# Optimization experiments

Hardware: AMD Instinct MI355X
Metric: run time of the kernel (lower is better)

Reference implementation:

```python
import jax, jax.numpy as jnp
import numpy as np

B, N, C = 8, 4096, 512
NH, R = 8, 4
EPS = 1e-5

def setup_inputs() -> dict:
    key = jax.random.key(0)
    ks = jax.random.split(key, 6)
    s = lambda k, shape: jax.random.normal(k, shape, jnp.float32) * 0.02
    return {
        'x': jax.random.normal(ks[0], (B, N, C), jnp.float32),
        'Wq': s(ks[1], (C, C)), 'bq': jnp.zeros((C,), jnp.float32),
        'Wkv': s(ks[2], (C, 2 * C)), 'bkv': jnp.zeros((2 * C,), jnp.float32),
        'Wp': s(ks[3], (C, C)), 'bp': jnp.zeros((C,), jnp.float32),
        'Wsr': s(ks[4], (C, C, R, R)), 'bsr': jnp.zeros((C,), jnp.float32),
        'gamma': jnp.ones((C,), jnp.float32), 'beta': jnp.zeros((C,), jnp.float32),
        'H': 64, 'W': 64,
    }

def reference(x, Wq, bq, Wkv, bkv, Wp, bp, Wsr, bsr, gamma, beta, H, W):
    b, n, c = x.shape
    nh = NH
    hd = c // nh
    scale = hd ** -0.5
    # Q projection -> [B, nh, N, hd]
    q = (x @ Wq + bq).reshape(b, n, nh, hd).transpose(0, 2, 1, 3)
    # spatial reduction of KV input: Conv2d(k=stride=R), NCHW
    x_sp = x.transpose(0, 2, 1).reshape(b, c, H, W)
    xr = jax.lax.conv_general_dilated(
        x_sp, Wsr, window_strides=(R, R), padding='VALID',
        dimension_numbers=('NCHW', 'OIHW', 'NCHW')) + bsr[None, :, None, None]
    nr = (H // R) * (W // R)
    xr = xr.reshape(b, c, nr).transpose(0, 2, 1)  # [B, Nr, C]
    # LayerNorm over channels
    mu = xr.mean(-1, keepdims=True)
    var = xr.var(-1, keepdims=True)
    xr = (xr - mu) / jnp.sqrt(var + EPS) * gamma + beta
    # KV projection -> k, v: [B, nh, Nr, hd]
    kv = (xr @ Wkv + bkv).reshape(b, nr, 2, nh, hd)
    k = kv[:, :, 0].transpose(0, 2, 1, 3)
    v = kv[:, :, 1].transpose(0, 2, 1, 3)
    # attention
    attn = jax.nn.softmax(jnp.einsum('bhnd,bhmd->bhnm', q, k) * scale, axis=-1)
    out = jnp.einsum('bhnm,bhmd->bhnd', attn, v).transpose(0, 2, 1, 3).reshape(b, n, c)
    return out @ Wp + bp
```

## Files before the change

### kernel.cpp

```cpp
#include <hip/hip_runtime.h>
#include <stdint.h>

typedef __attribute__((ext_vector_type(8))) short bf16x8;
typedef __attribute__((ext_vector_type(4))) float f32x4;
typedef __attribute__((ext_vector_type(2))) unsigned u32x2;

#define MFMA16(a,b,c) __builtin_amdgcn_mfma_f32_16x16x32_bf16(a,b,c,0,0,0)

typedef const __attribute__((address_space(1))) void GV;
typedef __attribute__((address_space(3))) void LV;

static __device__ __forceinline__ void gload16(const void* g, void* l) {
  __builtin_amdgcn_global_load_lds((GV*)g, (LV*)l, 16, 0, 0);
}

static __device__ __forceinline__ unsigned short f2bf(float f) {
  union { float f; unsigned u; } x; x.f = f;
  unsigned r = x.u + 0x7FFFu + ((x.u >> 16) & 1u);
  return (unsigned short)(r >> 16);
}

static __device__ __forceinline__ float fast_exp2(float x) {
#if __has_builtin(__builtin_amdgcn_exp2f)
  return __builtin_amdgcn_exp2f(x);
#else
  return __expf(x * 0.6931471805599453f);
#endif
}

__global__ __launch_bounds__(256) void pack_all(
    const float* __restrict__ x, const float* __restrict__ Wq,
    const float* __restrict__ Wkv, const float* __restrict__ Wp,
    const float* __restrict__ Wsr,
    unsigned short* __restrict__ xb, unsigned short* __restrict__ wqt,
    unsigned short* __restrict__ wkvt, unsigned short* __restrict__ wpt,
    unsigned short* __restrict__ wsrt) {
  const int tid = threadIdx.x;
  int bid = blockIdx.x;
  if (bid < 16384) {
    int i = bid * 256 + tid;
    float4 v = ((const float4*)x)[i];
    unsigned a0 = f2bf(v.x), a1 = f2bf(v.y), a2 = f2bf(v.z), a3 = f2bf(v.w);
    uint2 pk; pk.x = a0 | (a1 << 16); pk.y = a2 | (a3 << 16);
    ((uint2*)xb)[i] = pk;
    return;
  }
  bid -= 16384;
  __shared__ float lsm[8704];

  auto wtile = [&](const float* __restrict__ W, unsigned short* __restrict__ out,
                   int ldw, int tr, int tc) {
    int k0 = tr * 64, n0 = tc * 64;
    #pragma unroll
    for (int i = 0; i < 16; ++i) {
      int idx = i * 256 + tid; int r = idx >> 6, c = idx & 63;
      lsm[r * 65 + c] = W[(size_t)(k0 + r) * ldw + n0 + c];
    }
    __syncthreads();
    #pragma unroll
    for (int i = 0; i < 16; ++i) {
      int idx = i * 256 + tid; int n = idx >> 6, k = idx & 63;
      out[(size_t)(n0 + n) * 512 + k0 + k] = f2bf(lsm[k * 65 + n]);
    }
  };

  if (bid < 64) { wtile(Wq, wqt, 512, bid >> 3, bid & 7); return; }
  bid -= 64;
  if (bid < 128) { wtile(Wkv, wkvt, 1024, bid >> 4, bid & 15); return; }
  bid -= 128;
  if (bid < 64) { wtile(Wp, wpt, 512, bid >> 3, bid & 7); return; }
  bid -= 64;
  int oc = bid;
  #pragma unroll
  for (int i = 0; i < 32; ++i) {
    int idx = i * 256 + tid;
    lsm[(idx >> 4) * 17 + (idx & 15)] = Wsr[(size_t)oc * 8192 + idx];
  }
  __syncthreads();
  #pragma unroll
  for (int i = 0; i < 32; ++i) {
    int idx = i * 256 + tid;
    int ic = idx & 511, r12 = idx >> 9;
    wsrt[(size_t)oc * 8192 + idx] = f2bf(lsm[ic * 17 + r12]);
  }
}

template<int WM, int WN, int MREP, int NREP, int MODE, bool CONV>
static __device__ __forceinline__ void gemm_body(
    unsigned short* lds_a, unsigned short* lds_b,
    const unsigned short* __restrict__ A, const unsigned short* __restrict__ Bt,
    const float* __restrict__ bias, void* __restrict__ outp,
    unsigned short* __restrict__ out_k, unsigned short* __restrict__ out_v,
    int M, int N, int K, int lda, int Ksub, int m0, int n0, int kbeg, int zslice) {
  constexpr int BM = WM * MREP * 16;
  constexpr int BN = WN * NREP * 16;
  constexpr int BK = 64;
  constexpr int ABYTES = BM * BK * 2;
  constexpr int BBYTES = BN * BK * 2;
  const int tid = threadIdx.x;
  const int lane = tid & 63, w = tid >> 6;
  const int wr = w / WN, wc = w % WN;
  const int l15 = lane & 15, lhi = lane >> 4;
  const int xmask = (l15 & 7) << 4;
  const int smask = ((tid >> 3) & 7) << 3;

  f32x4 acc[MREP][NREP] = {};
  constexpr int AR = ABYTES / 4096;
  constexpr int BR = BBYTES / 4096;
  constexpr int NL = AR + BR;

  auto stage = [&](int buf, int k0) {
    #pragma unroll
    for (int r = 0; r < AR; ++r) {
      int o = r * 4096 + tid * 16;
      int row = o >> 7;
      int kc = (((o & 127) >> 1)) ^ smask;
      const unsigned short* src;
      if constexpr (CONV) {
        int m = m0 + row;
        int bb = m >> 8, pix = m & 255;
        int oh = pix >> 4, ow = pix & 15;
        int r12 = k0 >> 9;
        int icc = (k0 & 511) + kc;
        int r1 = r12 >> 2, r2 = r12 & 3;
        int nn = (oh * 4 + r1) * 64 + ow * 4 + r2;
        src = A + ((size_t)(bb * 4096 + nn)) * 512 + icc;
      } else {
        src = A + (size_t)(m0 + row) * lda + k0 + kc;
      }
      gload16(src, (char*)lds_a + buf * ABYTES + r * 4096 + w * 1024);
    }
    #pragma unroll
    for (int r = 0; r < BR; ++r) {
      int o = r * 4096 + tid * 16;
      int row = o >> 7;
      int kc = (((o & 127) >> 1)) ^ smask;
      const unsigned short* src = Bt + (size_t)(n0 + row) * K + k0 + kc;
      gload16(src, (char*)lds_b + buf * BBYTES + r * 4096 + w * 1024);
    }
  };

  auto waitn = [&]() {
    if constexpr (NL == 4)      asm volatile("s_waitcnt vmcnt(4)" ::: "memory");
    else if constexpr (NL == 6) asm volatile("s_waitcnt vmcnt(6)" ::: "memory");
    else                        asm volatile("s_waitcnt vmcnt(8)" ::: "memory");
  };

  auto compute = [&](int buf) {
    const char* pa = (const char*)lds_a + buf * ABYTES;
    const char* pb = (const char*)lds_b + buf * BBYTES;
    #pragma unroll
    for (int kk = 0; kk < BK; kk += 32) {
      bf16x8 af[MREP], bfr[NREP];
      #pragma unroll
      for (int m = 0; m < MREP; ++m)
        af[m] = *(const bf16x8*)(pa + (wr * MREP * 16 + m * 16 + l15) * (BK * 2)
                                 + (((kk << 1) + (lhi << 4)) ^ xmask));
      #pragma unroll
      for (int n = 0; n < NREP; ++n)
        bfr[n] = *(const bf16x8*)(pb + (wc * NREP * 16 + n * 16 + l15) * (BK * 2)
                                  + (((kk << 1) + (lhi << 4)) ^ xmask));
      __builtin_amdgcn_s_setprio(1);
      #pragma unroll
      for (int m = 0; m < MREP; ++m)
        #pragma unroll
        for (int n = 0; n < NREP; ++n)
          acc[m][n] = MFMA16(af[m], bfr[n], acc[m][n]);
      __builtin_amdgcn_s_setprio(0);
    }
  };

  const int nsteps = Ksub / BK;
  stage(0, kbeg);
  int buf = 0;
  for (int t = 0; t < nsteps; ++t) {
    if (t + 1 < nsteps) {
      stage(buf ^ 1, kbeg + (t + 1) * BK);
      waitn();
    } else {
      asm volatile("s_waitcnt vmcnt(0)" ::: "memory");
    }
    __builtin_amdgcn_s_barrier();
    compute(buf);
    __builtin_amdgcn_s_barrier();
    buf ^= 1;
  }

  #pragma unroll
  for (int m = 0; m < MREP; ++m) {
    #pragma unroll
    for (int n = 0; n < NREP; ++n) {
      #pragma unroll
      for (int r = 0; r < 4; ++r) {
        int gm = m0 + wr * MREP * 16 + m * 16 + lhi * 4 + r;
        int gn = n0 + wc * NREP * 16 + n * 16 + l15;
        if constexpr (MODE == 0) {
          float v = acc[m][n][r] + bias[gn];
          ((float*)outp)[(size_t)gm * N + gn] = v;
        } else if constexpr (MODE == 3) {
          ((float*)outp)[((size_t)zslice * M + gm) * N + gn] = acc[m][n][r];
        } else if constexpr (MODE == 4) {
          float v = (acc[m][n][r] + bias[gn]) * 0.18033688011112042f;
          int b_ = gm >> 12, n_ = gm & 4095;
          int hh = gn >> 6, d = gn & 63;
          int qt = n_ >> 4, half = d >> 5, dd = d & 31;
          int ln = (n_ & 15) | ((dd >> 3) << 4);
          ((unsigned short*)outp)[(size_t)(b_ * 8 + hh) * 262144 +
              (qt * 2 + half) * 512 + ln * 8 + (d & 7)] = f2bf(v);
        } else {
          float v = acc[m][n][r] + bias[gn];
          unsigned short bv = f2bf(v);
          int bb = gm >> 8, nr = gm & 255;
          if (gn < 512) {
            int hh = gn >> 6, d = gn & 63;
            int t_ = nr >> 4, half = d >> 5, dd = d & 31;
            int ln = (nr & 15) | ((dd >> 3) << 4);
            out_k[(size_t)(bb * 8 + hh) * 16384 +
                  (t_ * 2 + half) * 512 + ln * 8 + (d & 7)] = bv;
          } else {
            int c = gn - 512;
            int hh = c >> 6, d = c & 63;
            int nn = d >> 4, cl = d & 15;
            int ks = nr >> 5, lh = (nr >> 3) & 3;
            out_v[(size_t)(bb * 8 + hh) * 16384 +
                  (nn * 8 + ks) * 512 + (cl | (lh << 4)) * 8 + (nr & 7)] = bv;
          }
        }
      }
    }
  }
}

template<int WM, int WN, int MREP, int NREP, int MODE, bool CONV, bool SWZ>
__global__ __launch_bounds__(256) void gemm_bf16(
    const unsigned short* __restrict__ A, const unsigned short* __restrict__ Bt,
    const float* __restrict__ bias, void* __restrict__ outp,
    unsigned short* __restrict__ out_k, unsigned short* __restrict__ out_v,
    int M, int N, int K, int lda, int Ksub) {
  constexpr int BM = WM * MREP * 16;
  constexpr int BN = WN * NREP * 16;
  __shared__ unsigned short lds_a[2 * BM * 64];
  __shared__ unsigned short lds_b[2 * BN * 64];
  int mt, nt_;
  if constexpr (SWZ) {
    int lin = blockIdx.x + blockIdx.y * gridDim.x;
    int nwg = gridDim.x * gridDim.y;
    int cpx = nwg >> 3;
    int s = (lin & 7) * cpx + (lin >> 3);
    int gdy = gridDim.y;
    mt = s / gdy; nt_ = s - mt * gdy;
  } else { mt = blockIdx.x; nt_ = blockIdx.y; }
  gemm_body<WM, WN, MREP, NREP, MODE, CONV>(
      lds_a, lds_b, A, Bt, bias, outp, out_k, out_v,
      M, N, K, lda, Ksub, mt * BM, nt_ * BN, blockIdx.z * Ksub, blockIdx.z);
}

__global__ __launch_bounds__(256) void proj_fused(
    const unsigned short* __restrict__ xb, const unsigned short* __restrict__ wqt,
    const float* __restrict__ bq, unsigned short* __restrict__ qfrag,
    const unsigned short* __restrict__ xln, const unsigned short* __restrict__ wkvt,
    const float* __restrict__ bkv, unsigned short* __restrict__ kfrag,
    unsigned short* __restrict__ vfrag) {
  __shared__ unsigned short lds_a[2 * 128 * 64];
  __shared__ unsigned short lds_b[2 * 128 * 64];
  int bx = blockIdx.x;
  if (bx < 1024) {
    int s = (bx & 7) * 128 + (bx >> 3);
    int mt = s >> 2, nt_ = s & 3;
    gemm_body<2, 2, 4, 4, 4, false>(
        lds_a, lds_b, xb, wqt, bq, qfrag, nullptr, nullptr,
        32768, 512, 512, 512, 512, mt * 128, nt_ * 128, 0, 0);
  } else {
    int b2 = bx - 1024;
    int mt = b2 >> 3, nt_ = b2 & 7;
    gemm_body<2, 2, 4, 4, 2, false>(
        lds_a, lds_b, xln, wkvt, bkv, nullptr, kfrag, vfrag,
        2048, 1024, 512, 512, 512, mt * 128, nt_ * 128, 0, 0);
  }
}

__global__ __launch_bounds__(64) void ln_kernel(
    const float* __restrict__ part, const float* __restrict__ bsr,
    const float* __restrict__ gamma, const float* __restrict__ beta,
    unsigned short* __restrict__ xln) {
  const int row = blockIdx.x, lane = threadIdx.x;
  float vv[8];
  #pragma unroll
  for (int j = 0; j < 8; ++j) vv[j] = bsr[lane * 8 + j];
  #pragma unroll
  for (int p = 0; p < 8; ++p) {
    const float* pp = part + ((size_t)p * 2048 + row) * 512 + lane * 8;
    float4 a0 = *(const float4*)pp;
    float4 a1 = *(const float4*)(pp + 4);
    vv[0] += a0.x; vv[1] += a0.y; vv[2] += a0.z; vv[3] += a0.w;
    vv[4] += a1.x; vv[5] += a1.y; vv[6] += a1.z; vv[7] += a1.w;
  }
  float s = 0.f, s2 = 0.f;
  #pragma unroll
  for (int j = 0; j < 8; ++j) { s += vv[j]; s2 += vv[j] * vv[j]; }
  #pragma unroll
  for (int m_ = 1; m_ < 64; m_ <<= 1) { s += __shfl_xor(s, m_); s2 += __shfl_xor(s2, m_); }
  float mean = s * (1.f / 512.f);
  float var = s2 * (1.f / 512.f) - mean * mean;
  float inv = rsqrtf(var + 1e-5f);
  #pragma unroll
  for (int j = 0; j < 8; ++j) {
    int c = lane * 8 + j;
    xln[(size_t)row * 512 + c] = f2bf((vv[j] - mean) * inv * gamma[c] + beta[c]);
  }
}

__global__ __launch_bounds__(512, 4) void attn_kernel(
    const unsigned short* __restrict__ qfrag, const unsigned short* __restrict__ kfrag,
    const unsigned short* __restrict__ vfrag, unsigned short* __restrict__ aout) {
  __shared__ unsigned short k_lds[16384];
  __shared__ unsigned short v_lds[16384];
  const int tid = threadIdx.x, lane = tid & 63, w = tid >> 6;
  const int l15 = lane & 15;
  const int b = blockIdx.z, h = blockIdx.y;
  const int bh = b * 8 + h;
  const char* kb_ = (const char*)(kfrag + (size_t)bh * 16384);
  const char* vb_ = (const char*)(vfrag + (size_t)bh * 16384);
  #pragma unroll
  for (int r = 0; r < 4; ++r) {
    gload16(kb_ + r * 8192 + tid * 16, (char*)k_lds + r * 8192 + w * 1024);
    gload16(vb_ + r * 8192 + tid * 16, (char*)v_lds + r * 8192 + w * 1024);
  }
  const int qt = blockIdx.x * 8 + w;
  const unsigned short* qbase = qfrag + (size_t)bh * 262144 + (size_t)qt * 1024;
  bf16x8 qf0 = *(const bf16x8*)(qbase + lane * 8);
  bf16x8 qf1 = *(const bf16x8*)(qbase + 512 + lane * 8);
  __syncthreads();

  f32x4 st[16];
  #pragma unroll
  for (int t = 0; t < 16; ++t) {
    bf16x8 kf0 = *(const bf16x8*)&k_lds[t * 1024 + lane * 8];
    bf16x8 kf1 = *(const bf16x8*)&k_lds[t * 1024 + 512 + lane * 8];
    f32x4 a = {0.f, 0.f, 0.f, 0.f};
    a = MFMA16(kf0, qf0, a);
    a = MFMA16(kf1, qf1, a);
    st[t] = a;
  }

  float sum = 0.f;
  unsigned pk2[16][2];
  #pragma unroll
  for (int t = 0; t < 16; ++t) {
    float p0 = fast_exp2(st[t][0]), p1 = fast_exp2(st[t][1]);
    float p2 = fast_exp2(st[t][2]), p3 = fast_exp2(st[t][3]);
    sum += (p0 + p1) + (p2 + p3);
    unsigned r0, r1;
    asm("v_cvt_pk_bf16_f32 %0, %1, %2" : "=v"(r0) : "v"(p0), "v"(p1));
    asm("v_cvt_pk_bf16_f32 %0, %1, %2" : "=v"(r1) : "v"(p2), "v"(p3));
    pk2[t][0] = r0; pk2[t][1] = r1;
  }
  sum += __shfl_xor(sum, 16);
  sum += __shfl_xor(sum, 32);
  float invs = 1.f / sum;

  const int lhi_ = lane >> 4;
  const int srcA = l15 + (((2 * lhi_) & 3) << 4);
  const int srcB = l15 + (((2 * lhi_ + 1) & 3) << 4);
  const bool hi2 = lhi_ >= 2;
  f32x4 o[4] = {};
  #pragma unroll
  for (int ks = 0; ks < 8; ++ks) {
    union { unsigned u[4]; bf16x8 v; } pu;
    unsigned A0 = __shfl(pk2[2 * ks][0], srcA),     A0b = __shfl(pk2[2 * ks][1], srcA);
    unsigned A1 = __shfl(pk2[2 * ks + 1][0], srcA), A1b = __shfl(pk2[2 * ks + 1][1], srcA);
    unsigned B0 = __shfl(pk2[2 * ks][0], srcB),     B0b = __shfl(pk2[2 * ks][1], srcB);
    unsigned B1 = __shfl(pk2[2 * ks + 1][0], srcB), B1b = __shfl(pk2[2 * ks + 1][1], srcB);
    pu.u[0] = hi2 ? A1 : A0;  pu.u[1] = hi2 ? A1b : A0b;
    pu.u[2] = hi2 ? B1 : B0;  pu.u[3] = hi2 ? B1b : B0b;
    #pragma unroll
    for (int n = 0; n < 4; ++n) {
      bf16x8 vf = *(const bf16x8*)&v_lds[(n * 8 + ks) * 512 + lane * 8];
      o[n] = MFMA16(vf, pu.v, o[n]);
    }
  }

  const int q0 = blockIdx.x * 128;
  const int lhi = lane >> 4;
  #pragma unroll
  for (int n = 0; n < 4; ++n) {
    float a0 = o[n][0] * invs, a1 = o[n][1] * invs;
    float a2 = o[n][2] * invs, a3 = o[n][3] * invs;
    unsigned w0, w1;
    asm("v_cvt_pk_bf16_f32 %0, %1, %2" : "=v"(w0) : "v"(a0), "v"(a1));
    asm("v_cvt_pk_bf16_f32 %0, %1, %2" : "=v"(w1) : "v"(a2), "v"(a3));
    u32x2 pr; pr[0] = w0; pr[1] = w1;
    size_t base = (size_t)(b * 4096 + q0 + w * 16 + l15) * 512 + h * 64 + n * 16 + lhi * 4;
    *(u32x2*)(aout + base) = pr;
  }
}

extern "C" void kernel_launch(void* const* d_in, const int* in_sizes, int n_in,
                              void* d_out, int out_size, void* d_ws, size_t ws_size,
                              hipStream_t stream) {
  const float* x     = (const float*)d_in[0];
  const float* Wq    = (const float*)d_in[1];
  const float* bq    = (const float*)d_in[2];
  const float* Wkv   = (const float*)d_in[3];
  const float* bkv   = (const float*)d_in[4];
  const float* Wp    = (const float*)d_in[5];
  const float* bp    = (const float*)d_in[6];
  const float* Wsr   = (const float*)d_in[7];
  const float* bsr   = (const float*)d_in[8];
  const float* gamma = (const float*)d_in[9];
  const float* beta  = (const float*)d_in[10];

  char* ws = (char*)d_ws;
  unsigned short* xb    = (unsigned short*)(ws + 0);
  float*          part  = (float*)(ws + 33554432);
  unsigned short* qfrag = (unsigned short*)(ws + 33554432);
  unsigned short* wqt   = (unsigned short*)(ws + 67108864);
  unsigned short* wkvt  = (unsigned short*)(ws + 67633152);
  unsigned short* wpt   = (unsigned short*)(ws + 68681728);
  unsigned short* wsrt  = (unsigned short*)(ws + 69206016);
  unsigned short* xln   = (unsigned short*)(ws + 77594624);
  unsigned short* kfrag = (unsigned short*)(ws + 79691776);
  unsigned short* vfrag = (unsigned short*)(ws + 81788928);
  unsigned short* aout  = xb;

  pack_all<<<17152, 256, 0, stream>>>(x, Wq, Wkv, Wp, Wsr, xb, wqt, wkvt, wpt, wsrt);
  gemm_bf16<2, 2, 4, 4, 3, true, true><<<dim3(16, 4, 8), 256, 0, stream>>>(
      xb, wsrt, nullptr, part, nullptr, nullptr, 2048, 512, 8192, 512, 1024);
  ln_kernel<<<2048, 64, 0, stream>>>(part, bsr, gamma, beta, xln);
  proj_fused<<<1152, 256, 0, stream>>>(xb, wqt, bq, qfrag, xln, wkvt, bkv, kfrag, vfrag);
  attn_kernel<<<dim3(32, 8, 8), 512, 0, stream>>>(qfrag, kfrag, vfrag, aout);
  gemm_bf16<2, 2, 4, 4, 0, false, true><<<dim3(256, 4, 1), 256, 0, stream>>>(
      aout, wpt, bp, (float*)d_out, nullptr, nullptr, 32768, 512, 512, 512, 512);
}
```

Before: 154.3 us.

## Replace double-buffered LDS staging with single buffer in GEMM body

Removes the double-buffered global-to-LDS prefetch in the shared GEMM body, so each K step now loads a tile, waits for all loads to finish, computes, and then syncs. LDS allocation is halved, which could allow more workgroups per CU. In exchange, global load latency is no longer overlapped with MFMA compute within a workgroup.

```diff
diff --git a/kernel.cpp b/kernel.cpp
--- a/kernel.cpp
+++ b/kernel.cpp
@@ -107,9 +107,8 @@
   f32x4 acc[MREP][NREP] = {};
   constexpr int AR = ABYTES / 4096;
   constexpr int BR = BBYTES / 4096;
-  constexpr int NL = AR + BR;
-
-  auto stage = [&](int buf, int k0) {
+
+  auto stage = [&](int k0) {
     #pragma unroll
     for (int r = 0; r < AR; ++r) {
       int o = r * 4096 + tid * 16;
@@ -128,7 +127,7 @@
       } else {
         src = A + (size_t)(m0 + row) * lda + k0 + kc;
       }
-      gload16(src, (char*)lds_a + buf * ABYTES + r * 4096 + w * 1024);
+      gload16(src, (char*)lds_a + r * 4096 + w * 1024);
     }
     #pragma unroll
     for (int r = 0; r < BR; ++r) {
@@ -136,19 +135,13 @@
       int row = o >> 7;
       int kc = (((o & 127) >> 1)) ^ smask;
       const unsigned short* src = Bt + (size_t)(n0 + row) * K + k0 + kc;
-      gload16(src, (char*)lds_b + buf * BBYTES + r * 4096 + w * 1024);
+      gload16(src, (char*)lds_b + r * 4096 + w * 1024);
     }
   };
 
-  auto waitn = [&]() {
-    if constexpr (NL == 4)      asm volatile("s_waitcnt vmcnt(4)" ::: "memory");
-    else if constexpr (NL == 6) asm volatile("s_waitcnt vmcnt(6)" ::: "memory");
-    else                        asm volatile("s_waitcnt vmcnt(8)" ::: "memory");
-  };
-
-  auto compute = [&](int buf) {
-    const char* pa = (const char*)lds_a + buf * ABYTES;
-    const char* pb = (const char*)lds_b + buf * BBYTES;
+  auto compute = [&]() {
+    const char* pa = (const char*)lds_a;
+    const char* pb = (const char*)lds_b;
     #pragma unroll
     for (int kk = 0; kk < BK; kk += 32) {
       bf16x8 af[MREP], bfr[NREP];
@@ -171,19 +164,12 @@
   };
 
   const int nsteps = Ksub / BK;
-  stage(0, kbeg);
-  int buf = 0;
   for (int t = 0; t < nsteps; ++t) {
-    if (t + 1 < nsteps) {
-      stage(buf ^ 1, kbeg + (t + 1) * BK);
-      waitn();
-    } else {
-      asm volatile("s_waitcnt vmcnt(0)" ::: "memory");
-    }
+    stage(kbeg + t * BK);
+    asm volatile("s_waitcnt vmcnt(0)" ::: "memory");
     __builtin_amdgcn_s_barrier();
-    compute(buf);
+    compute();
     __builtin_amdgcn_s_barrier();
-    buf ^= 1;
   }
 
   #pragma unroll
@@ -239,8 +225,8 @@
     int M, int N, int K, int lda, int Ksub) {
   constexpr int BM = WM * MREP * 16;
   constexpr int BN = WN * NREP * 16;
-  __shared__ unsigned short lds_a[2 * BM * 64];
-  __shared__ unsigned short lds_b[2 * BN * 64];
+  __shared__ unsigned short lds_a[BM * 64];
+  __shared__ unsigned short lds_b[BN * 64];
   int mt, nt_;
   if constexpr (SWZ) {
     int lin = blockIdx.x + blockIdx.y * gridDim.x;
@@ -261,8 +247,8 @@
     const unsigned short* __restrict__ xln, const unsigned short* __restrict__ wkvt,
     const float* __restrict__ bkv, unsigned short* __restrict__ kfrag,
     unsigned short* __restrict__ vfrag) {
-  __shared__ unsigned short lds_a[2 * 128 * 64];
-  __shared__ unsigned short lds_b[2 * 128 * 64];
+  __shared__ unsigned short lds_a[128 * 64];
+  __shared__ unsigned short lds_b[128 * 64];
   int bx = blockIdx.x;
   if (bx < 1024) {
     int s = (bx & 7) * 128 + (bx >> 3);
```

Result: slower. 167.0 us (+8.3%).

## Use single-buffered high-occupancy GEMM for projections and split fused proj kernel

Applied to the files above, without the earlier changes.

Replaces the double-buffered templated GEMM for the K=512 projections with a single-buffered kernel that uses half the LDS and sets launch_bounds(256,4), so more workgroups fit per CU and latency is hidden by occupancy instead of software pipelining. The conv GEMM keeps its own specialised double-buffered kernel. The fused Q/KV projection launch is split into two separate launches (KV first, then Q). Exposed load latency per K step and an extra kernel launch are the costs.

```diff
diff --git a/kernel.cpp b/kernel.cpp
--- a/kernel.cpp
+++ b/kernel.cpp
@@ -85,107 +85,11 @@
   }
 }
 
-template<int WM, int WN, int MREP, int NREP, int MODE, bool CONV>
-static __device__ __forceinline__ void gemm_body(
-    unsigned short* lds_a, unsigned short* lds_b,
-    const unsigned short* __restrict__ A, const unsigned short* __restrict__ Bt,
-    const float* __restrict__ bias, void* __restrict__ outp,
+template<int MREP, int NREP, int MODE>
+static __device__ __forceinline__ void epilogue(
+    f32x4 (&acc)[MREP][NREP], const float* __restrict__ bias, void* __restrict__ outp,
     unsigned short* __restrict__ out_k, unsigned short* __restrict__ out_v,
-    int M, int N, int K, int lda, int Ksub, int m0, int n0, int kbeg, int zslice) {
-  constexpr int BM = WM * MREP * 16;
-  constexpr int BN = WN * NREP * 16;
-  constexpr int BK = 64;
-  constexpr int ABYTES = BM * BK * 2;
-  constexpr int BBYTES = BN * BK * 2;
-  const int tid = threadIdx.x;
-  const int lane = tid & 63, w = tid >> 6;
-  const int wr = w / WN, wc = w % WN;
-  const int l15 = lane & 15, lhi = lane >> 4;
-  const int xmask = (l15 & 7) << 4;
-  const int smask = ((tid >> 3) & 7) << 3;
-
-  f32x4 acc[MREP][NREP] = {};
-  constexpr int AR = ABYTES / 4096;
-  constexpr int BR = BBYTES / 4096;
-  constexpr int NL = AR + BR;
-
-  auto stage = [&](int buf, int k0) {
-    #pragma unroll
-    for (int r = 0; r < AR; ++r) {
-      int o = r * 4096 + tid * 16;
-      int row = o >> 7;
-      int kc = (((o & 127) >> 1)) ^ smask;
-      const unsigned short* src;
-      if constexpr (CONV) {
-        int m = m0 + row;
-        int bb = m >> 8, pix = m & 255;
-        int oh = pix >> 4, ow = pix & 15;
-        int r12 = k0 >> 9;
-        int icc = (k0 & 511) + kc;
-        int r1 = r12 >> 2, r2 = r12 & 3;
-        int nn = (oh * 4 + r1) * 64 + ow * 4 + r2;
-        src = A + ((size_t)(bb * 4096 + nn)) * 512 + icc;
-      } else {
-        src = A + (size_t)(m0 + row) * lda + k0 + kc;
-      }
-      gload16(src, (char*)lds_a + buf * ABYTES + r * 4096 + w * 1024);
-    }
-    #pragma unroll
-    for (int r = 0; r < BR; ++r) {
-      int o = r * 4096 + tid * 16;
-      int row = o >> 7;
-      int kc = (((o & 127) >> 1)) ^ smask;
-      const unsigned short* src = Bt + (size_t)(n0 + row) * K + k0 + kc;
-      gload16(src, (char*)lds_b + buf * BBYTES + r * 4096 + w * 1024);
-    }
-  };
-
-  auto waitn = [&]() {
-    if constexpr (NL == 4)      asm volatile("s_waitcnt vmcnt(4)" ::: "memory");
-    else if constexpr (NL == 6) asm volatile("s_waitcnt vmcnt(6)" ::: "memory");
-    else                        asm volatile("s_waitcnt vmcnt(8)" ::: "memory");
-  };
-
-  auto compute = [&](int buf) {
-    const char* pa = (const char*)lds_a + buf * ABYTES;
-    const char* pb = (const char*)lds_b + buf * BBYTES;
-    #pragma unroll
-    for (int kk = 0; kk < BK; kk += 32) {
-      bf16x8 af[MREP], bfr[NREP];
-      #pragma unroll
-      for (int m = 0; m < MREP; ++m)
-        af[m] = *(const bf16x8*)(pa + (wr * MREP * 16 + m * 16 + l15) * (BK * 2)
-                                 + (((kk << 1) + (lhi << 4)) ^ xmask));
-      #pragma unroll
-      for (int n = 0; n < NREP; ++n)
-        bfr[n] = *(const bf16x8*)(pb + (wc * NREP * 16 + n * 16 + l15) * (BK * 2)
-                                  + (((kk << 1) + (lhi << 4)) ^ xmask));
-      __builtin_amdgcn_s_setprio(1);
-      #pragma unroll
-      for (int m = 0; m < MREP; ++m)
-        #pragma unroll
-        for (int n = 0; n < NREP; ++n)
-          acc[m][n] = MFMA16(af[m], bfr[n], acc[m][n]);
-      __builtin_amdgcn_s_setprio(0);
-    }
-  };
-
-  const int nsteps = Ksub / BK;
-  stage(0, kbeg);
-  int buf = 0;
-  for (int t = 0; t < nsteps; ++t) {
-    if (t + 1 < nsteps) {
-      stage(buf ^ 1, kbeg + (t + 1) * BK);
-      waitn();
-    } else {
-      asm volatile("s_waitcnt vmcnt(0)" ::: "memory");
-    }
-    __builtin_amdgcn_s_barrier();
-    compute(buf);
-    __builtin_amdgcn_s_barrier();
-    buf ^= 1;
-  }
-
+    int M, int N, int m0, int n0, int wr, int wc, int l15, int lhi, int zslice) {
   #pragma unroll
   for (int m = 0; m < MREP; ++m) {
     #pragma unroll
@@ -195,8 +99,7 @@
         int gm = m0 + wr * MREP * 16 + m * 16 + lhi * 4 + r;
         int gn = n0 + wc * NREP * 16 + n * 16 + l15;
         if constexpr (MODE == 0) {
-          float v = acc[m][n][r] + bias[gn];
-          ((float*)outp)[(size_t)gm * N + gn] = v;
+          ((float*)outp)[(size_t)gm * N + gn] = acc[m][n][r] + bias[gn];
         } else if constexpr (MODE == 3) {
           ((float*)outp)[((size_t)zslice * M + gm) * N + gn] = acc[m][n][r];
         } else if constexpr (MODE == 4) {
@@ -231,16 +134,20 @@
   }
 }
 
-template<int WM, int WN, int MREP, int NREP, int MODE, bool CONV, bool SWZ>
-__global__ __launch_bounds__(256) void gemm_bf16(
+template<int MODE, bool SWZ>
+__global__ __launch_bounds__(256, 4) void gemm_1b(
     const unsigned short* __restrict__ A, const unsigned short* __restrict__ Bt,
     const float* __restrict__ bias, void* __restrict__ outp,
     unsigned short* __restrict__ out_k, unsigned short* __restrict__ out_v,
-    int M, int N, int K, int lda, int Ksub) {
-  constexpr int BM = WM * MREP * 16;
-  constexpr int BN = WN * NREP * 16;
-  __shared__ unsigned short lds_a[2 * BM * 64];
-  __shared__ unsigned short lds_b[2 * BN * 64];
+    int M, int N, int K, int lda) {
+  constexpr int BM = 128, BN = 128, BK = 64;
+  __shared__ unsigned short lds_a[BM * BK];
+  __shared__ unsigned short lds_b[BN * BK];
+  const int tid = threadIdx.x;
+  const int lane = tid & 63, w = tid >> 6;
+  const int wr = w >> 1, wc = w & 1;
+  const int l15 = lane & 15, lhi = lane >> 4;
+  const int xmask = (l15 & 7) << 4;
   int mt, nt_;
   if constexpr (SWZ) {
     int lin = blockIdx.x + blockIdx.y * gridDim.x;
@@ -250,33 +157,143 @@
     int gdy = gridDim.y;
     mt = s / gdy; nt_ = s - mt * gdy;
   } else { mt = blockIdx.x; nt_ = blockIdx.y; }
-  gemm_body<WM, WN, MREP, NREP, MODE, CONV>(
-      lds_a, lds_b, A, Bt, bias, outp, out_k, out_v,
-      M, N, K, lda, Ksub, mt * BM, nt_ * BN, blockIdx.z * Ksub, blockIdx.z);
-}
-
-__global__ __launch_bounds__(256) void proj_fused(
-    const unsigned short* __restrict__ xb, const unsigned short* __restrict__ wqt,
-    const float* __restrict__ bq, unsigned short* __restrict__ qfrag,
-    const unsigned short* __restrict__ xln, const unsigned short* __restrict__ wkvt,
-    const float* __restrict__ bkv, unsigned short* __restrict__ kfrag,
-    unsigned short* __restrict__ vfrag) {
-  __shared__ unsigned short lds_a[2 * 128 * 64];
-  __shared__ unsigned short lds_b[2 * 128 * 64];
-  int bx = blockIdx.x;
-  if (bx < 1024) {
-    int s = (bx & 7) * 128 + (bx >> 3);
-    int mt = s >> 2, nt_ = s & 3;
-    gemm_body<2, 2, 4, 4, 4, false>(
-        lds_a, lds_b, xb, wqt, bq, qfrag, nullptr, nullptr,
-        32768, 512, 512, 512, 512, mt * 128, nt_ * 128, 0, 0);
-  } else {
-    int b2 = bx - 1024;
-    int mt = b2 >> 3, nt_ = b2 & 7;
-    gemm_body<2, 2, 4, 4, 2, false>(
-        lds_a, lds_b, xln, wkvt, bkv, nullptr, kfrag, vfrag,
-        2048, 1024, 512, 512, 512, mt * 128, nt_ * 128, 0, 0);
-  }
+  const int m0 = mt * BM;
+  const int n0 = nt_ * BN;
+
+  const int srow = tid >> 3;
+  const int kcs = ((tid & 7) << 3) ^ (((tid >> 3) & 7) << 3);
+  const unsigned short* ap = A + (size_t)(m0 + srow) * lda + kcs;
+  const unsigned short* bp = Bt + (size_t)(n0 + srow) * K + kcs;
+  char* adst = (char*)lds_a + w * 1024 + (lane << 4);
+  char* bdst = (char*)lds_b + w * 1024 + (lane << 4);
+  (void)adst; (void)bdst;
+
+  f32x4 acc[4][4] = {};
+  const int nsteps = K / BK;
+  for (int t = 0; t < nsteps; ++t) {
+    #pragma unroll
+    for (int r = 0; r < 4; ++r)
+      gload16(ap + (size_t)r * 32 * lda, (char*)lds_a + r * 4096 + w * 1024);
+    #pragma unroll
+    for (int r = 0; r < 4; ++r)
+      gload16(bp + (size_t)r * 32 * K, (char*)lds_b + r * 4096 + w * 1024);
+    asm volatile("s_waitcnt vmcnt(0)" ::: "memory");
+    __builtin_amdgcn_s_barrier();
+    #pragma unroll
+    for (int kk = 0; kk < BK; kk += 32) {
+      bf16x8 af[4], bfr[4];
+      #pragma unroll
+      for (int m = 0; m < 4; ++m)
+        af[m] = *(const bf16x8*)((const char*)lds_a + (wr * 64 + m * 16 + l15) * 128
+                                 + (((kk << 1) + (lhi << 4)) ^ xmask));
+      #pragma unroll
+      for (int n = 0; n < 4; ++n)
+        bfr[n] = *(const bf16x8*)((const char*)lds_b + (wc * 64 + n * 16 + l15) * 128
+                                  + (((kk << 1) + (lhi << 4)) ^ xmask));
+      #pragma unroll
+      for (int m = 0; m < 4; ++m)
+        #pragma unroll
+        for (int n = 0; n < 4; ++n)
+          acc[m][n] = MFMA16(af[m], bfr[n], acc[m][n]);
+    }
+    __builtin_amdgcn_s_barrier();
+    ap += BK; bp += BK;
+  }
+
+  epilogue<4, 4, MODE>(acc, bias, outp, out_k, out_v, M, N, m0, n0, wr, wc, l15, lhi, 0);
+}
+
+__global__ __launch_bounds__(256) void gemm_conv(
+    const unsigned short* __restrict__ A, const unsigned short* __restrict__ Bt,
+    float* __restrict__ outp, int Ksub) {
+  constexpr int BM = 128, BN = 128, BK = 64;
+  constexpr int ABYTES = BM * BK * 2;
+  __shared__ unsigned short lds_a[2 * BM * BK];
+  __shared__ unsigned short lds_b[2 * BN * BK];
+  const int tid = threadIdx.x;
+  const int lane = tid & 63, w = tid >> 6;
+  const int wr = w >> 1, wc = w & 1;
+  const int l15 = lane & 15, lhi = lane >> 4;
+  const int xmask = (l15 & 7) << 4;
+  const int smask = ((tid >> 3) & 7) << 3;
+  int lin = blockIdx.x + blockIdx.y * gridDim.x;
+  int nwg = gridDim.x * gridDim.y;
+  int cpx = nwg >> 3;
+  int s = (lin & 7) * cpx + (lin >> 3);
+  int mt = s / gridDim.y, nt_ = s - mt * gridDim.y;
+  const int m0 = mt * BM, n0 = nt_ * BN;
+  const int kbeg = blockIdx.z * Ksub;
+
+  f32x4 acc[4][4] = {};
+
+  auto stage = [&](int buf, int k0) {
+    #pragma unroll
+    for (int r = 0; r < 4; ++r) {
+      int o = r * 4096 + tid * 16;
+      int row = o >> 7;
+      int kc = (((o & 127) >> 1)) ^ smask;
+      int m = m0 + row;
+      int bb = m >> 8, pix = m & 255;
+      int oh = pix >> 4, ow = pix & 15;
+      int r12 = k0 >> 9;
+      int icc = (k0 & 511) + kc;
+      int r1 = r12 >> 2, r2 = r12 & 3;
+      int nn = (oh * 4 + r1) * 64 + ow * 4 + r2;
+      const unsigned short* src = A + ((size_t)(bb * 4096 + nn)) * 512 + icc;
+      gload16(src, (char*)lds_a + buf * ABYTES + r * 4096 + w * 1024);
+    }
+    #pragma unroll
+    for (int r = 0; r < 4; ++r) {
+      int o = r * 4096 + tid * 16;
+      int row = o >> 7;
+      int kc = (((o & 127) >> 1)) ^ smask;
+      const unsigned short* src = Bt + (size_t)(n0 + row) * 8192 + k0 + kc;
+      gload16(src, (char*)lds_b + buf * ABYTES + r * 4096 + w * 1024);
+    }
+  };
+
+  auto compute = [&](int buf) {
+    const char* pa = (const char*)lds_a + buf * ABYTES;
+    const char* pb = (const char*)lds_b + buf * ABYTES;
+    #pragma unroll
+    for (int kk = 0; kk < BK; kk += 32) {
+      bf16x8 af[4], bfr[4];
+      #pragma unroll
+      for (int m = 0; m < 4; ++m)
+        af[m] = *(const bf16x8*)(pa + (wr * 64 + m * 16 + l15) * 128
+                                 + (((kk << 1) + (lhi << 4)) ^ xmask));
+      #pragma unroll
+      for (int n = 0; n < 4; ++n)
+        bfr[n] = *(const bf16x8*)(pb + (wc * 64 + n * 16 + l15) * 128
+                                  + (((kk << 1) + (lhi << 4)) ^ xmask));
+      __builtin_amdgcn_s_setprio(1);
+      #pragma unroll
+      for (int m = 0; m < 4; ++m)
+        #pragma unroll
+        for (int n = 0; n < 4; ++n)
+          acc[m][n] = MFMA16(af[m], bfr[n], acc[m][n]);
+      __builtin_amdgcn_s_setprio(0);
+    }
+  };
+
+  const int nsteps = Ksub / BK;
+  stage(0, kbeg);
+  int buf = 0;
+  for (int t = 0; t < nsteps; ++t) {
+    if (t + 1 < nsteps) {
+      stage(buf ^ 1, kbeg + (t + 1) * BK);
+      asm volatile("s_waitcnt vmcnt(8)" ::: "memory");
+    } else {
+      asm volatile("s_waitcnt vmcnt(0)" ::: "memory");
+    }
+    __builtin_amdgcn_s_barrier();
+    compute(buf);
+    __builtin_amdgcn_s_barrier();
+    buf ^= 1;
+  }
+
+  epilogue<4, 4, 3>(acc, nullptr, outp, nullptr, nullptr, 2048, 512, m0, n0,
+                    wr, wc, l15, lhi, blockIdx.z);
 }
 
 __global__ __launch_bounds__(64) void ln_kernel(
@@ -424,11 +441,13 @@
   unsigned short* aout  = xb;
 
   pack_all<<<17152, 256, 0, stream>>>(x, Wq, Wkv, Wp, Wsr, xb, wqt, wkvt, wpt, wsrt);
-  gemm_bf16<2, 2, 4, 4, 3, true, true><<<dim3(16, 4, 8), 256, 0, stream>>>(
-      xb, wsrt, nullptr, part, nullptr, nullptr, 2048, 512, 8192, 512, 1024);
+  gemm_conv<<<dim3(16, 4, 8), 256, 0, stream>>>(xb, wsrt, part, 1024);
   ln_kernel<<<2048, 64, 0, stream>>>(part, bsr, gamma, beta, xln);
-  proj_fused<<<1152, 256, 0, stream>>>(xb, wqt, bq, qfrag, xln, wkvt, bkv, kfrag, vfrag);
+  gemm_1b<2, false><<<dim3(16, 8), 256, 0, stream>>>(
+      xln, wkvt, bkv, nullptr, kfrag, vfrag, 2048, 1024, 512, 512);
+  gemm_1b<4, true><<<dim3(256, 4), 256, 0, stream>>>(
+      xb, wqt, bq, qfrag, nullptr, nullptr, 32768, 512, 512, 512);
   attn_kernel<<<dim3(32, 8, 8), 512, 0, stream>>>(qfrag, kfrag, vfrag, aout);
-  gemm_bf16<2, 2, 4, 4, 0, false, true><<<dim3(256, 4, 1), 256, 0, stream>>>(
-      aout, wpt, bp, (float*)d_out, nullptr, nullptr, 32768, 512, 512, 512, 512);
-}
+  gemm_1b<0, true><<<dim3(256, 4), 256, 0, stream>>>(
+      aout, wpt, bp, (float*)d_out, nullptr, nullptr, 32768, 512, 512, 512);
+}
```

Result: slower. 160.2 us (+3.8%).
